# Kernel optimization log

Hardware: AMD Instinct MI355X
Metric: run time of the kernel (lower is better)

The kernel has to match this reference:

```python
import jax, jax.numpy as jnp
import numpy as np

N = 8192
D_IN = 6       # dim(concat(node, centre)) = 3 + 3
D_OUT = 512    # output_size


def setup_inputs() -> dict:
    key = jax.random.key(0)
    ks = jax.random.split(key, 9)
    s_in = 1.0 / np.sqrt(D_IN)
    s_v = 1.0 / np.sqrt(2 * D_OUT)
    return {
        "nodes": jax.random.normal(ks[0], (N, 3), dtype=jnp.float32),
        "centre": jax.random.normal(ks[1], (1, 3), dtype=jnp.float32),
        "Wq": jax.random.uniform(ks[2], (D_OUT, D_IN), jnp.float32, -s_in, s_in),
        "bq": jax.random.uniform(ks[3], (D_OUT,), jnp.float32, -s_in, s_in),
        "Wk": jax.random.uniform(ks[4], (D_OUT, D_IN), jnp.float32, -s_in, s_in),
        "bk": jax.random.uniform(ks[5], (D_OUT,), jnp.float32, -s_in, s_in),
        "Wv": jax.random.uniform(ks[6], (D_OUT, 2 * D_OUT), jnp.float32, -s_v, s_v),
        "bv": jax.random.uniform(ks[7], (D_OUT,), jnp.float32, -s_v, s_v),
    }


def reference(nodes, centre, Wq, bq, Wk, bk, Wv, bv):
    n = nodes.shape[0]
    d = Wv.shape[0]
    # x = concat(nodes, broadcast centre)  -> [N, 6]
    x = jnp.concatenate([nodes, jnp.broadcast_to(centre, (n, centre.shape[1]))], axis=1)
    keys = x @ Wk.T + bk          # [N, D]
    queries = x @ Wq.T + bq       # [N, D]
    attn = jax.nn.softmax(keys @ queries.T, axis=1)  # [N, N], rows sum to 1
    # values(concat(queries, keys[n])) decomposes linearly:
    #   V[n, m] = queries[m] @ Wv_q.T + keys[n] @ Wv_k.T + bv
    # so out[n] = attn[n] @ (queries @ Wv_q.T) + keys[n] @ Wv_k.T + bv
    Wv_q = Wv[:, :d]
    Wv_k = Wv[:, d:]
    out = attn @ (queries @ Wv_q.T) + keys @ Wv_k.T + bv
    return keys + out
```

## Files before the change

### kernel.cpp

```cpp
#include <hip/hip_runtime.h>

#define N_NODES 8192
#define DOUT    512
#define LOG2E   1.4426950408889634f
#define SQRT3   1.7320508075688772f

__device__ __forceinline__ float exp2_raw(float x) {
    float r;
    asm("v_exp_f32 %0, %1" : "=v"(r) : "v"(x));
    return r;
}


__global__ __launch_bounds__(64) void k2_tables_aux(
    const float* __restrict__ nodes, const float* __restrict__ centre,
    const float* __restrict__ Wq, const float* __restrict__ bq,
    const float* __restrict__ Wk, const float* __restrict__ bk,
    const float* __restrict__ Wv, const float* __restrict__ bv,
    float* __restrict__ T, float* __restrict__ aux)
{
    const int r = blockIdx.x, lane = threadIdx.x;
    const float c0 = centre[0], c1 = centre[1], c2 = centre[2];

    if (r < 512) {
        const float* wvq = Wv + (size_t)r * 1024;
        const float* wvk = wvq + 512;

        float m0=0.f,m1=0.f,m2=0.f,uc=0.f,r0=0.f,r1=0.f,r2=0.f,rc=0.f;
        for (int s = lane; s < 512; s += 64) {
            float a = wvq[s];
            float b = wvk[s];
            float kcs = fmaf(Wk[s*6+3], c0, fmaf(Wk[s*6+4], c1,
                        fmaf(Wk[s*6+5], c2, bk[s])));
            float us  = fmaf(Wq[s*6+3], c0, fmaf(Wq[s*6+4], c1,
                        fmaf(Wq[s*6+5], c2, bq[s])));
            m0 = fmaf(a, Wq[s*6+0], m0);
            m1 = fmaf(a, Wq[s*6+1], m1);
            m2 = fmaf(a, Wq[s*6+2], m2);
            uc = fmaf(a, us, uc);
            r0 = fmaf(b, Wk[s*6+0], r0);
            r1 = fmaf(b, Wk[s*6+1], r1);
            r2 = fmaf(b, Wk[s*6+2], r2);
            rc = fmaf(b, kcs, rc);
        }
        #pragma unroll
        for (int off = 32; off; off >>= 1) {
            m0 += __shfl_xor(m0, off); m1 += __shfl_xor(m1, off);
            m2 += __shfl_xor(m2, off); uc += __shfl_xor(uc, off);
            r0 += __shfl_xor(r0, off); r1 += __shfl_xor(r1, off);
            r2 += __shfl_xor(r2, off); rc += __shfl_xor(rc, off);
        }
        if (lane == 0) {
            float kcr = fmaf(Wk[r*6+3], c0, fmaf(Wk[r*6+4], c1,
                        fmaf(Wk[r*6+5], c2, bk[r])));
            T[r*8+0] = Wk[r*6+0] + r0;
            T[r*8+1] = Wk[r*6+1] + r1;
            T[r*8+2] = Wk[r*6+2] + r2;
            T[r*8+3] = kcr + rc + uc + bv[r];
            T[r*8+4] = m0; T[r*8+5] = m1; T[r*8+6] = m2; T[r*8+7] = 0.f;
        }
    } else if (r < 524) {
        const int o = r - 512;
        float acc = 0.f;
        if (o < 9) {
            int a = o / 3, b = o - a*3;
            for (int s = lane; s < 512; s += 64)
                acc = fmaf(Wq[s*6+a], Wk[s*6+b], acc);
        } else {
            int a = o - 9;
            for (int s = lane; s < 512; s += 64) {
                float kc = fmaf(Wk[s*6+3], c0, fmaf(Wk[s*6+4], c1,
                           fmaf(Wk[s*6+5], c2, bk[s])));
                acc = fmaf(Wq[s*6+a], kc, acc);
            }
        }
        #pragma unroll
        for (int off = 32; off; off >>= 1) acc += __shfl_xor(acc, off);
        if (lane == 0) aux[o] = acc * LOG2E;
    } else {
        const int b = r - 524;
        const float4* src = (const float4*)nodes + (size_t)b * 768;
        float m = 0.f;
        for (int k = lane; k < 768; k += 64) {
            float4 v = src[k];
            m = fmaxf(m, fmaxf(fmaxf(fabsf(v.x), fabsf(v.y)),
                               fmaxf(fabsf(v.z), fabsf(v.w))));
        }
        #pragma unroll
        for (int off = 32; off; off >>= 1) m = fmaxf(m, __shfl_xor(m, off));
        if (lane == 0) aux[12 + b] = m;
    }
}

__global__ __launch_bounds__(256) void k3_attn(
    const float* __restrict__ nodes,
    const float* __restrict__ aux, const float* __restrict__ T,
    float* __restrict__ out)
{
    __shared__ float lds[4096 * 3];
    const int tid = threadIdx.x, lane = tid & 63, wv = tid >> 6;
    const int ibase = (blockIdx.x * 4 + wv) * 4;

    const float G00=aux[0],G01=aux[1],G02=aux[2];
    const float G10=aux[3],G11=aux[4],G12=aux[5];
    const float G20=aux[6],G21=aux[7],G22=aux[8];
    const float g0=aux[9],g1=aux[10],g2=aux[11];
    float C = aux[12];
    #pragma unroll
    for (int b = 1; b < 8; ++b) C = fmaxf(C, aux[12+b]);
    const float Nbound = SQRT3 * C;

    float nx_[4], ny_[4], nz_[4], vx[4], vy[4], vz[4], bb[4];
    float S[4], ax[4], ay[4], az[4];
    #pragma unroll
    for (int q = 0; q < 4; ++q) {
        int i = ibase + q;
        float x = nodes[3*i], y = nodes[3*i+1], z = nodes[3*i+2];
        nx_[q]=x; ny_[q]=y; nz_[q]=z;
        float a = fmaf(G00,x, fmaf(G01,y, fmaf(G02,z, g0)));
        float b = fmaf(G10,x, fmaf(G11,y, fmaf(G12,z, g1)));
        float c = fmaf(G20,x, fmaf(G21,y, fmaf(G22,z, g2)));
        vx[q]=a; vy[q]=b; vz[q]=c;
        bb[q] = -sqrtf(fmaf(a,a, fmaf(b,b, c*c))) * Nbound;
        S[q]=0.f; ax[q]=0.f; ay[q]=0.f; az[q]=0.f;
    }

    for (int tile = 0; tile < 2; ++tile) {
        const float4* src = (const float4*)(nodes + tile*12288);
        float4* dst = (float4*)lds;
        for (int k = tid; k < 3072; k += 256) dst[k] = src[k];
        __syncthreads();
        for (int jj = lane; jj < 4096; jj += 128) {
            const int j2 = jj + 64;
            float nx0 = lds[jj*3+0], ny0 = lds[jj*3+1], nz0 = lds[jj*3+2];
            float nx1 = lds[j2*3+0], ny1 = lds[j2*3+1], nz1 = lds[j2*3+2];
            #pragma unroll
            for (int q = 0; q < 4; ++q) {
                float a0 = fmaf(vx[q],nx0, fmaf(vy[q],ny0, fmaf(vz[q],nz0, bb[q])));
                float a1 = fmaf(vx[q],nx1, fmaf(vy[q],ny1, fmaf(vz[q],nz1, bb[q])));
                float e0 = exp2_raw(a0);
                float e1 = exp2_raw(a1);
                S[q] += e0;
                ax[q] = fmaf(e0, nx0, ax[q]);
                ay[q] = fmaf(e0, ny0, ay[q]);
                az[q] = fmaf(e0, nz0, az[q]);
                S[q] += e1;
                ax[q] = fmaf(e1, nx1, ax[q]);
                ay[q] = fmaf(e1, ny1, ay[q]);
                az[q] = fmaf(e1, nz1, az[q]);
            }
        }
        __syncthreads();
    }

    #pragma unroll
    for (int q = 0; q < 4; ++q) {
        #pragma unroll
        for (int off = 32; off; off >>= 1) {
            S[q]  += __shfl_xor(S[q],  off);
            ax[q] += __shfl_xor(ax[q], off);
            ay[q] += __shfl_xor(ay[q], off);
            az[q] += __shfl_xor(az[q], off);
        }
        float inv = 1.f / fmaxf(S[q], 1e-35f);
        ax[q] *= inv; ay[q] *= inv; az[q] *= inv;
    }

    const float4* T4 = (const float4*)T;
    #pragma unroll
    for (int t = 0; t < 4; ++t) {
        int d0 = t*128 + lane*2;
        float4 A0 = T4[2*d0+0], B0 = T4[2*d0+1];
        float4 A1 = T4[2*d0+2], B1 = T4[2*d0+3];
        #pragma unroll
        for (int q = 0; q < 4; ++q) {
            float v0 = fmaf(A0.x,nx_[q], fmaf(A0.y,ny_[q], fmaf(A0.z,nz_[q],
                       fmaf(B0.x,ax[q], fmaf(B0.y,ay[q], fmaf(B0.z,az[q], A0.w))))));
            float v1 = fmaf(A1.x,nx_[q], fmaf(A1.y,ny_[q], fmaf(A1.z,nz_[q],
                       fmaf(B1.x,ax[q], fmaf(B1.y,ay[q], fmaf(B1.z,az[q], A1.w))))));
            *(float2*)(out + (size_t)(ibase+q)*DOUT + d0) = make_float2(v0, v1);
        }
    }
}

extern "C" void kernel_launch(void* const* d_in, const int* in_sizes, int n_in,
                              void* d_out, int out_size, void* d_ws, size_t ws_size,
                              hipStream_t stream) {
    const float* nodes  = (const float*)d_in[0];
    const float* centre = (const float*)d_in[1];
    const float* Wq     = (const float*)d_in[2];
    const float* bq     = (const float*)d_in[3];
    const float* Wk     = (const float*)d_in[4];
    const float* bk     = (const float*)d_in[5];
    const float* Wv     = (const float*)d_in[6];
    const float* bv     = (const float*)d_in[7];

    float* ws  = (float*)(((uintptr_t)d_ws + 255) & ~(uintptr_t)255);
    float* aux = ws;
    float* T   = ws + 32;
    float* out = (float*)d_out;

    hipLaunchKernelGGL(k2_tables_aux, dim3(532), dim3(64), 0, stream,
                       nodes, centre, Wq, bq, Wk, bk, Wv, bv, T, aux);
    hipLaunchKernelGGL(k3_attn,       dim3(512), dim3(256), 0, stream,
                       nodes, aux, T, out);
}
```

Measured before the change: 101.4 us.

## Transpose node tile to SoA in LDS, prefetch second tile, widen prep kernel

The attention kernel now writes each node tile into LDS as separate x/y/z planes, so each lane can read four nodes with one float4 load per coordinate instead of strided scalar loads. The global load of the second tile is issued into registers before the first tile is processed, overlapping that fetch with compute. Launch bounds ask for two blocks per CU. The table/aux kernel moves to 128 threads with a shared-memory cross-wave reduction and float2 weight loads. The trade-off is higher register pressure from the staged float4 arrays, which may cut occupancy.

```diff
diff --git a/kernel.cpp b/kernel.cpp
--- a/kernel.cpp
+++ b/kernel.cpp
@@ -12,14 +12,15 @@
 }
 
 
-__global__ __launch_bounds__(64) void k2_tables_aux(
+__global__ __launch_bounds__(128) void k2_tables_aux(
     const float* __restrict__ nodes, const float* __restrict__ centre,
     const float* __restrict__ Wq, const float* __restrict__ bq,
     const float* __restrict__ Wk, const float* __restrict__ bk,
     const float* __restrict__ Wv, const float* __restrict__ bv,
     float* __restrict__ T, float* __restrict__ aux)
 {
-    const int r = blockIdx.x, lane = threadIdx.x;
+    __shared__ float red[16];
+    const int r = blockIdx.x, tid = threadIdx.x, lane = tid & 63, wv = tid >> 6;
     const float c0 = centre[0], c1 = centre[1], c2 = centre[2];
 
     if (r < 512) {
@@ -27,20 +28,24 @@
         const float* wvk = wvq + 512;
 
         float m0=0.f,m1=0.f,m2=0.f,uc=0.f,r0=0.f,r1=0.f,r2=0.f,rc=0.f;
-        for (int s = lane; s < 512; s += 64) {
+        #pragma unroll
+        for (int it = 0; it < 4; ++it) {
+            int s = it*128 + tid;
             float a = wvq[s];
             float b = wvk[s];
-            float kcs = fmaf(Wk[s*6+3], c0, fmaf(Wk[s*6+4], c1,
-                        fmaf(Wk[s*6+5], c2, bk[s])));
-            float us  = fmaf(Wq[s*6+3], c0, fmaf(Wq[s*6+4], c1,
-                        fmaf(Wq[s*6+5], c2, bq[s])));
-            m0 = fmaf(a, Wq[s*6+0], m0);
-            m1 = fmaf(a, Wq[s*6+1], m1);
-            m2 = fmaf(a, Wq[s*6+2], m2);
+            const float2* wk2 = (const float2*)(Wk + s*6);
+            const float2* wq2 = (const float2*)(Wq + s*6);
+            float2 k01 = wk2[0], k23 = wk2[1], k45 = wk2[2];
+            float2 q01 = wq2[0], q23 = wq2[1], q45 = wq2[2];
+            float kcs = fmaf(k23.y, c0, fmaf(k45.x, c1, fmaf(k45.y, c2, bk[s])));
+            float us  = fmaf(q23.y, c0, fmaf(q45.x, c1, fmaf(q45.y, c2, bq[s])));
+            m0 = fmaf(a, q01.x, m0);
+            m1 = fmaf(a, q01.y, m1);
+            m2 = fmaf(a, q23.x, m2);
             uc = fmaf(a, us, uc);
-            r0 = fmaf(b, Wk[s*6+0], r0);
-            r1 = fmaf(b, Wk[s*6+1], r1);
-            r2 = fmaf(b, Wk[s*6+2], r2);
+            r0 = fmaf(b, k01.x, r0);
+            r1 = fmaf(b, k01.y, r1);
+            r2 = fmaf(b, k23.x, r2);
             rc = fmaf(b, kcs, rc);
         }
         #pragma unroll
@@ -51,24 +56,37 @@
             r2 += __shfl_xor(r2, off); rc += __shfl_xor(rc, off);
         }
         if (lane == 0) {
+            float* q = red + wv*8;
+            q[0]=m0; q[1]=m1; q[2]=m2; q[3]=uc; q[4]=r0; q[5]=r1; q[6]=r2; q[7]=rc;
+        }
+        __syncthreads();
+        if (tid == 0) {
             float kcr = fmaf(Wk[r*6+3], c0, fmaf(Wk[r*6+4], c1,
                         fmaf(Wk[r*6+5], c2, bk[r])));
-            T[r*8+0] = Wk[r*6+0] + r0;
-            T[r*8+1] = Wk[r*6+1] + r1;
-            T[r*8+2] = Wk[r*6+2] + r2;
-            T[r*8+3] = kcr + rc + uc + bv[r];
-            T[r*8+4] = m0; T[r*8+5] = m1; T[r*8+6] = m2; T[r*8+7] = 0.f;
+            T[r*8+0] = Wk[r*6+0] + red[4] + red[12];
+            T[r*8+1] = Wk[r*6+1] + red[5] + red[13];
+            T[r*8+2] = Wk[r*6+2] + red[6] + red[14];
+            T[r*8+3] = kcr + red[7] + red[15] + red[3] + red[11] + bv[r];
+            T[r*8+4] = red[0] + red[8];
+            T[r*8+5] = red[1] + red[9];
+            T[r*8+6] = red[2] + red[10];
+            T[r*8+7] = 0.f;
         }
     } else if (r < 524) {
         const int o = r - 512;
         float acc = 0.f;
         if (o < 9) {
             int a = o / 3, b = o - a*3;
-            for (int s = lane; s < 512; s += 64)
+            #pragma unroll
+            for (int it = 0; it < 4; ++it) {
+                int s = it*128 + tid;
                 acc = fmaf(Wq[s*6+a], Wk[s*6+b], acc);
+            }
         } else {
             int a = o - 9;
-            for (int s = lane; s < 512; s += 64) {
+            #pragma unroll
+            for (int it = 0; it < 4; ++it) {
+                int s = it*128 + tid;
                 float kc = fmaf(Wk[s*6+3], c0, fmaf(Wk[s*6+4], c1,
                            fmaf(Wk[s*6+5], c2, bk[s])));
                 acc = fmaf(Wq[s*6+a], kc, acc);
@@ -76,28 +94,85 @@
         }
         #pragma unroll
         for (int off = 32; off; off >>= 1) acc += __shfl_xor(acc, off);
-        if (lane == 0) aux[o] = acc * LOG2E;
+        if (lane == 0) red[wv] = acc;
+        __syncthreads();
+        if (tid == 0) aux[o] = (red[0] + red[1]) * LOG2E;
     } else {
         const int b = r - 524;
         const float4* src = (const float4*)nodes + (size_t)b * 768;
         float m = 0.f;
-        for (int k = lane; k < 768; k += 64) {
-            float4 v = src[k];
+        #pragma unroll
+        for (int it = 0; it < 6; ++it) {
+            float4 v = src[it*128 + tid];
             m = fmaxf(m, fmaxf(fmaxf(fabsf(v.x), fabsf(v.y)),
                                fmaxf(fabsf(v.z), fabsf(v.w))));
         }
         #pragma unroll
         for (int off = 32; off; off >>= 1) m = fmaxf(m, __shfl_xor(m, off));
-        if (lane == 0) aux[12 + b] = m;
-    }
-}
-
-__global__ __launch_bounds__(256) void k3_attn(
+        if (lane == 0) red[wv] = m;
+        __syncthreads();
+        if (tid == 0) aux[12 + b] = fmaxf(red[0], red[1]);
+    }
+}
+
+
+__device__ __forceinline__ void stage_load(const float4* __restrict__ src, int tid,
+                                           float4 v[4][3]) {
+    #pragma unroll
+    for (int k = 0; k < 4; ++k) {
+        int t = k*256 + tid;
+        v[k][0] = src[t*3+0];
+        v[k][1] = src[t*3+1];
+        v[k][2] = src[t*3+2];
+    }
+}
+
+__device__ __forceinline__ void stage_write(float* __restrict__ lds, int tid,
+                                            float4 v[4][3]) {
+    #pragma unroll
+    for (int k = 0; k < 4; ++k) {
+        int t = k*256 + tid;
+        float4 a = v[k][0], b = v[k][1], c = v[k][2];
+        *(float4*)&lds[        t*4] = make_float4(a.x, a.w, b.z, c.y);
+        *(float4*)&lds[4096 +  t*4] = make_float4(a.y, b.x, b.w, c.z);
+        *(float4*)&lds[8192 +  t*4] = make_float4(a.z, b.y, c.x, c.w);
+    }
+}
+
+__device__ __forceinline__ void attn_tile(const float* __restrict__ lds, int lane,
+    const float vx[4], const float vy[4], const float vz[4], const float bb[4],
+    float S[4], float ax[4], float ay[4], float az[4])
+{
+    #pragma unroll 2
+    for (int it = 0; it < 16; ++it) {
+        int jj = it*256 + lane*4;
+        float4 X = *(const float4*)&lds[jj];
+        float4 Y = *(const float4*)&lds[4096 + jj];
+        float4 Z = *(const float4*)&lds[8192 + jj];
+        #pragma unroll
+        for (int q = 0; q < 4; ++q) {
+            float a0 = fmaf(vx[q],X.x, fmaf(vy[q],Y.x, fmaf(vz[q],Z.x, bb[q])));
+            float a1 = fmaf(vx[q],X.y, fmaf(vy[q],Y.y, fmaf(vz[q],Z.y, bb[q])));
+            float a2 = fmaf(vx[q],X.z, fmaf(vy[q],Y.z, fmaf(vz[q],Z.z, bb[q])));
+            float a3 = fmaf(vx[q],X.w, fmaf(vy[q],Y.w, fmaf(vz[q],Z.w, bb[q])));
+            float e0 = exp2_raw(a0);
+            float e1 = exp2_raw(a1);
+            float e2 = exp2_raw(a2);
+            float e3 = exp2_raw(a3);
+            S[q] += e0; ax[q]=fmaf(e0,X.x,ax[q]); ay[q]=fmaf(e0,Y.x,ay[q]); az[q]=fmaf(e0,Z.x,az[q]);
+            S[q] += e1; ax[q]=fmaf(e1,X.y,ax[q]); ay[q]=fmaf(e1,Y.y,ay[q]); az[q]=fmaf(e1,Z.y,az[q]);
+            S[q] += e2; ax[q]=fmaf(e2,X.z,ax[q]); ay[q]=fmaf(e2,Y.z,ay[q]); az[q]=fmaf(e2,Z.z,az[q]);
+            S[q] += e3; ax[q]=fmaf(e3,X.w,ax[q]); ay[q]=fmaf(e3,Y.w,ay[q]); az[q]=fmaf(e3,Z.w,az[q]);
+        }
+    }
+}
+
+__global__ __launch_bounds__(256, 2) void k3_attn(
     const float* __restrict__ nodes,
     const float* __restrict__ aux, const float* __restrict__ T,
     float* __restrict__ out)
 {
-    __shared__ float lds[4096 * 3];
+    __shared__ float lds[12288];
     const int tid = threadIdx.x, lane = tid & 63, wv = tid >> 6;
     const int ibase = (blockIdx.x * 4 + wv) * 4;
 
@@ -125,33 +200,16 @@
         S[q]=0.f; ax[q]=0.f; ay[q]=0.f; az[q]=0.f;
     }
 
-    for (int tile = 0; tile < 2; ++tile) {
-        const float4* src = (const float4*)(nodes + tile*12288);
-        float4* dst = (float4*)lds;
-        for (int k = tid; k < 3072; k += 256) dst[k] = src[k];
-        __syncthreads();
-        for (int jj = lane; jj < 4096; jj += 128) {
-            const int j2 = jj + 64;
-            float nx0 = lds[jj*3+0], ny0 = lds[jj*3+1], nz0 = lds[jj*3+2];
-            float nx1 = lds[j2*3+0], ny1 = lds[j2*3+1], nz1 = lds[j2*3+2];
-            #pragma unroll
-            for (int q = 0; q < 4; ++q) {
-                float a0 = fmaf(vx[q],nx0, fmaf(vy[q],ny0, fmaf(vz[q],nz0, bb[q])));
-                float a1 = fmaf(vx[q],nx1, fmaf(vy[q],ny1, fmaf(vz[q],nz1, bb[q])));
-                float e0 = exp2_raw(a0);
-                float e1 = exp2_raw(a1);
-                S[q] += e0;
-                ax[q] = fmaf(e0, nx0, ax[q]);
-                ay[q] = fmaf(e0, ny0, ay[q]);
-                az[q] = fmaf(e0, nz0, az[q]);
-                S[q] += e1;
-                ax[q] = fmaf(e1, nx1, ax[q]);
-                ay[q] = fmaf(e1, ny1, ay[q]);
-                az[q] = fmaf(e1, nz1, az[q]);
-            }
-        }
-        __syncthreads();
-    }
+    float4 s0[4][3], s1[4][3];
+    stage_load((const float4*)nodes, tid, s0);
+    stage_write(lds, tid, s0);
+    stage_load((const float4*)(nodes + 12288), tid, s1);
+    __syncthreads();
+    attn_tile(lds, lane, vx, vy, vz, bb, S, ax, ay, az);
+    __syncthreads();
+    stage_write(lds, tid, s1);
+    __syncthreads();
+    attn_tile(lds, lane, vx, vy, vz, bb, S, ax, ay, az);
 
     #pragma unroll
     for (int q = 0; q < 4; ++q) {
@@ -200,7 +258,7 @@
     float* T   = ws + 32;
     float* out = (float*)d_out;
 
-    hipLaunchKernelGGL(k2_tables_aux, dim3(532), dim3(64), 0, stream,
+    hipLaunchKernelGGL(k2_tables_aux, dim3(532), dim3(128), 0, stream,
                        nodes, centre, Wq, bq, Wk, bk, Wv, bv, T, aux);
     hipLaunchKernelGGL(k3_attn,       dim3(512), dim3(256), 0, stream,
                        nodes, aux, T, out);
```

Measured after the change: 96.53 us. -4.8%, faster.
